# Performance work log

Measured on AMD Instinct MI355X. Metric: run time of the kernel, lower is better.

Reference implementation:

```python
import jax, jax.numpy as jnp
import numpy as np

N_NODES = 1000      # nodes per graph
B = 64              # graphs in batch
N = B * N_NODES     # total nodes
E = 2048000         # total edges
F_IN, D1, D2 = 128, 256, 64


def setup_inputs() -> dict:
    key = jax.random.key(0)
    ks = jax.random.split(key, 24)
    def p(k, shape, fan_in):
        return jax.random.normal(k, shape, dtype=jnp.float32) * (1.0 / np.sqrt(fan_in))
    inp = {
        "x": jax.random.normal(ks[0], (N, F_IN), dtype=jnp.float32),
        "edge_index": jax.random.randint(ks[1], (2, E), 0, N, dtype=jnp.int32).astype(jnp.int64),
        "edge_attr": jax.random.uniform(ks[2], (E,), dtype=jnp.float32),
        # GraphConv1: lin_rel (neighbors) and lin_root (self)
        "Wl1": p(ks[3], (D1, F_IN), F_IN), "bl1": jnp.zeros((D1,), jnp.float32),
        "Wr1": p(ks[4], (D1, F_IN), F_IN), "br1": jnp.zeros((D1,), jnp.float32),
        # GraphConv2
        "Wl2": p(ks[5], (D2, D1), D1), "bl2": jnp.zeros((D2,), jnp.float32),
        "Wr2": p(ks[6], (D2, D1), D1), "br2": jnp.zeros((D2,), jnp.float32),
        # bottleneck fc / fc2
        "Wfc": p(ks[7], (D2, N_NODES * D2), N_NODES * D2), "bfc": jnp.zeros((D2,), jnp.float32),
        "Wfc2": p(ks[8], (N_NODES * D2, D2), D2), "bfc2": jnp.zeros((N_NODES * D2,), jnp.float32),
        # concatDec MLP: Linear(2*D2 -> D1) -> relu -> Linear(D1 -> 1)
        "Wd1": p(ks[9], (D1, 2 * D2), 2 * D2), "bd1": jnp.zeros((D1,), jnp.float32),
        "Wd2": p(ks[10], (1, D1), D1), "bd2": jnp.zeros((1,), jnp.float32),
    }
    return inp


def _graph_conv(x, src, dst, ew, Wl, bl, Wr, br):
    # PyG GraphConv: out = lin_rel(sum_{j in N(i)} w_ij * x_j) + lin_root(x_i)
    m = x[src] * ew[:, None]                       # [E, F] gather + scale
    agg = jax.ops.segment_sum(m, dst, num_segments=N)  # scatter-add to targets
    return agg @ Wl.T + bl + x @ Wr.T + br


def reference(x, edge_index, edge_attr,
              Wl1, bl1, Wr1, br1, Wl2, bl2, Wr2, br2,
              Wfc, bfc, Wfc2, bfc2, Wd1, bd1, Wd2, bd2):
    src = edge_index[0]
    dst = edge_index[1]
    # encode (dropout_adj / Dropout are identity at inference)
    h = jax.nn.relu(_graph_conv(x, src, dst, edge_attr, Wl1, bl1, Wr1, br1))
    z = _graph_conv(h, src, dst, edge_attr, Wl2, bl2, Wr2, br2)   # [N, D2]
    z = jax.nn.relu(z.reshape(-1, N_NODES * D2))                   # [B, N_NODES*D2]
    z = z @ Wfc.T + bfc                                            # [B, D2]
    # decode
    z = jax.nn.relu(z @ Wfc2.T + bfc2)                             # [B, N_NODES*D2]
    z = z.reshape(-1, D2)                                          # [N, D2]
    # concatDec over edges
    h_e = jnp.concatenate([z[src], z[dst]], axis=1)                # [E, 2*D2]
    h_e = jax.nn.relu(h_e @ Wd1.T + bd1)                           # [E, D1]
    pred = (h_e @ Wd2.T + bd2).reshape(-1)                         # [E]
    return jax.nn.sigmoid(pred)
```

## Files before the change

kernel.cpp:

```cpp
#include <hip/hip_runtime.h>
#include <math.h>

typedef __attribute__((ext_vector_type(8))) _Float16 f16x8;
typedef __attribute__((ext_vector_type(4))) _Float16 f16x4;
typedef __attribute__((ext_vector_type(2))) _Float16 f16x2;
typedef __attribute__((ext_vector_type(4))) float f32x4;

static __device__ __forceinline__ int getidx(const int* __restrict__ ei, int mode, long long pos) {
  return mode ? ei[2 * pos] : ei[pos];
}

__global__ void detect_kernel(const int* __restrict__ ei, int* __restrict__ mode) {
  int lane = threadIdx.x & 63;
  int v = ei[2 * lane + 1] | ei[2 * lane + 129];
  unsigned long long nz = __ballot(v != 0);
  if (lane == 0) mode[0] = (nz == 0ull) ? 1 : 0;
}

__global__ void zero_kernel(float* __restrict__ p, long long n) {
  long long i = (long long)blockIdx.x * blockDim.x + threadIdx.x;
  if (i < n) p[i] = 0.f;
}

__global__ void f32tof16_kernel(const float* __restrict__ in, unsigned short* __restrict__ out,
                                long long n4) {
  long long i = (long long)blockIdx.x * 256 + threadIdx.x;
  if (i >= n4) return;
  float4 v = ((const float4*)in)[i];
  f16x4 h;
  h[0] = (_Float16)v.x; h[1] = (_Float16)v.y; h[2] = (_Float16)v.z; h[3] = (_Float16)v.w;
  ((f16x4*)out)[i] = h;
}

__global__ void w16cat_kernel(const float* __restrict__ Wl1, const float* __restrict__ Wr1,
                              const float* __restrict__ Wl2, const float* __restrict__ Wr2,
                              unsigned short* __restrict__ wh1, unsigned short* __restrict__ wh2) {
  int idx = blockIdx.x * 256 + threadIdx.x;
  if (idx < 65536) {
    int o = idx >> 8, k = idx & 255;
    float v = (k < 128) ? Wl1[o * 128 + k] : Wr1[o * 128 + k - 128];
    _Float16 hv = (_Float16)v;
    wh1[idx] = *(unsigned short*)&hv;
  } else if (idx < 65536 + 32768) {
    int i2 = idx - 65536;
    int o = i2 >> 8, k = i2 & 255;
    float v = (o < 64) ? Wl2[o * 256 + k] : Wr2[(o - 64) * 256 + k];
    _Float16 hv = (_Float16)v;
    wh2[i2] = *(unsigned short*)&hv;
  }
}

__global__ void hist_kernel(const int* __restrict__ ei, int* __restrict__ cnt,
                            const int* __restrict__ modep, int E) {
  const int md = modep[0];
  int e = blockIdx.x * 256 + threadIdx.x;
  if (e >= E) return;
  int d = getidx(ei, md, (long long)E + e);
  atomicAdd(&cnt[d], 1);
}

__global__ void scan1_kernel(const int* __restrict__ cnt, int* __restrict__ pre,
                             int* __restrict__ bsum, int N) {
  __shared__ int ws[4];
  int i = blockIdx.x * 256 + threadIdx.x;
  int v = (i < N) ? cnt[i] : 0;
  int lane = threadIdx.x & 63, w = threadIdx.x >> 6;
  int s = v;
#pragma unroll
  for (int o = 1; o < 64; o <<= 1) { int t = __shfl_up(s, o); if (lane >= o) s += t; }
  if (lane == 63) ws[w] = s;
  __syncthreads();
  int off = 0;
  for (int k = 0; k < w; ++k) off += ws[k];
  if (i < N) pre[i] = s + off - v;
  if (threadIdx.x == 255) bsum[blockIdx.x] = s + off;
}

__global__ void scan2_kernel(int* __restrict__ bsum, int nb) {
  __shared__ int ws[4];
  int i = threadIdx.x;
  int v = (i < nb) ? bsum[i] : 0;
  int lane = i & 63, w = i >> 6;
  int s = v;
#pragma unroll
  for (int o = 1; o < 64; o <<= 1) { int t = __shfl_up(s, o); if (lane >= o) s += t; }
  if (lane == 63) ws[w] = s;
  __syncthreads();
  int off = 0;
  for (int k = 0; k < w; ++k) off += ws[k];
  if (i < nb) bsum[i] = s + off - v;
}

__global__ void scan3_kernel(int* __restrict__ rowptr, const int* __restrict__ bsum,
                             int* __restrict__ fill, int N, int E) {
  int i = blockIdx.x * 256 + threadIdx.x;
  if (i < N) {
    int r = rowptr[i] + bsum[blockIdx.x];
    rowptr[i] = r;
    fill[i] = r;
  }
  if (i == 0) rowptr[N] = E;
}

__global__ void reorder_kernel(const int* __restrict__ ei, const float* __restrict__ ea,
                               int* __restrict__ fill, uint4* __restrict__ se2,
                               const int* __restrict__ modep, int E) {
  const int md = modep[0];
  int e = blockIdx.x * 256 + threadIdx.x;
  if (e >= E) return;
  int s = getidx(ei, md, e);
  int d = getidx(ei, md, (long long)E + e);
  int pos = atomicAdd(&fill[d], 1);
  se2[pos] = make_uint4((unsigned)s, __float_as_uint(ea[e]), (unsigned)e, (unsigned)d);
}

__global__ void agg1_csr_kernel(const int* __restrict__ rowptr, const uint4* __restrict__ se2,
                                const unsigned short* __restrict__ xh,
                                unsigned short* __restrict__ agg1h, int N) {
  int n = (int)((blockIdx.x * 256 + threadIdx.x) >> 6);
  int lane = threadIdx.x & 63;
  if (n >= N) return;
  int p = rowptr[n], end = rowptr[n + 1];
  float ax = 0.f, ay = 0.f;
  for (; p + 1 < end; p += 2) {
    uint4 e0 = se2[p], e1 = se2[p + 1];
    float w0 = __uint_as_float(e0.y), w1 = __uint_as_float(e1.y);
    f16x2 v0 = *(const f16x2*)&xh[(size_t)e0.x * 128 + lane * 2];
    f16x2 v1 = *(const f16x2*)&xh[(size_t)e1.x * 128 + lane * 2];
    ax += (float)v0[0] * w0 + (float)v1[0] * w1;
    ay += (float)v0[1] * w0 + (float)v1[1] * w1;
  }
  if (p < end) {
    uint4 e0 = se2[p];
    float w0 = __uint_as_float(e0.y);
    f16x2 v0 = *(const f16x2*)&xh[(size_t)e0.x * 128 + lane * 2];
    ax += (float)v0[0] * w0;
    ay += (float)v0[1] * w0;
  }
  f16x2 st; st[0] = (_Float16)ax; st[1] = (_Float16)ay;
  *(f16x2*)&agg1h[(size_t)n * 128 + lane * 2] = st;
}

__global__ void agg2_csr_kernel(const int* __restrict__ rowptr, const uint4* __restrict__ se2,
                                const unsigned short* __restrict__ th, float* __restrict__ agg2,
                                int N) {
  int n = (int)((blockIdx.x * 256 + threadIdx.x) >> 6);
  int lane = threadIdx.x & 63;
  if (n >= N) return;
  int p = rowptr[n], end = rowptr[n + 1];
  float acc = 0.f;
  for (; p + 1 < end; p += 2) {
    uint4 e0 = se2[p], e1 = se2[p + 1];
    _Float16 t0 = *(const _Float16*)&th[(size_t)e0.x * 64 + lane];
    _Float16 t1 = *(const _Float16*)&th[(size_t)e1.x * 64 + lane];
    acc += (float)t0 * __uint_as_float(e0.y) + (float)t1 * __uint_as_float(e1.y);
  }
  if (p < end) {
    uint4 e0 = se2[p];
    _Float16 t0 = *(const _Float16*)&th[(size_t)e0.x * 64 + lane];
    acc += (float)t0 * __uint_as_float(e0.y);
  }
  agg2[(size_t)n * 64 + lane] += acc;
}

__global__ void scatter1_kernel(const int* __restrict__ ei, const float* __restrict__ ea,
                                const float* __restrict__ x, float* __restrict__ agg1,
                                const int* __restrict__ modep, int E) {
  const int md = modep[0];
  int e = (int)(((long long)blockIdx.x * 256 + threadIdx.x) >> 6);
  int lane = threadIdx.x & 63;
  if (e >= E) return;
  int s = getidx(ei, md, e);
  int d = getidx(ei, md, (long long)E + e);
  float w = ea[e];
  float2 v = *(const float2*)&x[(size_t)s * 128 + lane * 2];
  float* ap = &agg1[(size_t)d * 128 + lane * 2];
  atomicAdd(ap, v.x * w);
  atomicAdd(ap + 1, v.y * w);
}

__global__ void scatter2_kernel(const int* __restrict__ ei, const float* __restrict__ ea,
                                const float* __restrict__ t, float* __restrict__ agg2,
                                const int* __restrict__ modep, int E) {
  const int md = modep[0];
  int e = (int)(((long long)blockIdx.x * 256 + threadIdx.x) >> 6);
  int lane = threadIdx.x & 63;
  if (e >= E) return;
  int s = getidx(ei, md, e);
  int d = getidx(ei, md, (long long)E + e);
  float w = ea[e];
  atomicAdd(&agg2[(size_t)d * 64 + lane], t[(size_t)s * 64 + lane] * w);
}

__global__ void gemm_bt(const float* __restrict__ A1, const float* __restrict__ W1, int K1,
                        const float* __restrict__ A2, const float* __restrict__ W2, int K2,
                        const float* __restrict__ b1, const float* __restrict__ b2,
                        float* __restrict__ C, int NC, int doRelu) {
  __shared__ float As[64][17];
  __shared__ float Ws[64][17];
  int tid = threadIdx.x;
  int tx = tid & 15, ty = tid >> 4;
  int row0 = blockIdx.y * 64, col0 = blockIdx.x * 64;
  float acc[4][4] = {};
  for (int srcsel = 0; srcsel < 2; ++srcsel) {
    const float* A = srcsel ? A2 : A1;
    const float* W = srcsel ? W2 : W1;
    int K = srcsel ? K2 : K1;
    if (!A) continue;
    for (int kb = 0; kb < K; kb += 16) {
#pragma unroll
      for (int i = 0; i < 4; ++i) {
        int idx = tid + 256 * i;
        int r = idx >> 4, k = idx & 15;
        As[r][k] = A[(size_t)(row0 + r) * K + kb + k];
        Ws[r][k] = W[(size_t)(col0 + r) * K + kb + k];
      }
      __syncthreads();
#pragma unroll
      for (int k = 0; k < 16; ++k) {
        float a[4], w[4];
#pragma unroll
        for (int i = 0; i < 4; ++i) a[i] = As[ty * 4 + i][k];
#pragma unroll
        for (int j = 0; j < 4; ++j) w[j] = Ws[tx * 4 + j][k];
#pragma unroll
        for (int i = 0; i < 4; ++i)
#pragma unroll
          for (int j = 0; j < 4; ++j) acc[i][j] += a[i] * w[j];
      }
      __syncthreads();
    }
  }
#pragma unroll
  for (int j = 0; j < 4; ++j) {
    int c = col0 + tx * 4 + j;
    float bias = (b1 ? b1[c] : 0.f) + (b2 ? b2[c] : 0.f);
#pragma unroll
    for (int i = 0; i < 4; ++i) {
      float v = acc[i][j] + bias;
      if (doRelu) v = fmaxf(v, 0.f);
      C[(size_t)(row0 + ty * 4 + i) * NC + c] = v;
    }
  }
}

template <int MODE, int OTN>
__global__ void __launch_bounds__(256, 2)
gemm16_kernel(const uint4* __restrict__ A0, const uint4* __restrict__ A1, int c0,
              const unsigned short* __restrict__ Wcat,
              const float* __restrict__ b1, const float* __restrict__ b2,
              unsigned short* __restrict__ outH, float* __restrict__ outF) {
  __shared__ uint4 At[64 * 33];
  int tid = threadIdx.x;
  int lane = tid & 63;
  int wv = tid >> 6;
  int l15 = lane & 15, g = lane >> 4;
  int row0 = blockIdx.x * 64;

  f16x8 bfr[OTN][8];
  float biasv[OTN];
#pragma unroll
  for (int ot = 0; ot < OTN; ++ot) {
    int o = wv * (OTN * 16) + ot * 16 + l15;
    if (MODE == 0) biasv[ot] = b1[o] + b2[o];
    else biasv[ot] = (o >= 64) ? (b1[o - 64] + b2[o - 64]) : 0.f;
#pragma unroll
    for (int kb = 0; kb < 8; ++kb)
      bfr[ot][kb] = *(const f16x8*)&Wcat[(size_t)o * 256 + kb * 32 + g * 8];
  }

#pragma unroll
  for (int i = 0; i < 8; ++i) {
    int idx = tid + 256 * i;
    int r = idx >> 5, c = idx & 31;
    uint4 v = (c < c0) ? A0[(size_t)(row0 + r) * c0 + c]
                       : A1[(size_t)(row0 + r) * (32 - c0) + (c - c0)];
    At[r * 33 + c] = v;
  }
  __syncthreads();

#pragma unroll
  for (int est = 0; est < 4; ++est) {
    int rowA = est * 16 + l15;
    f16x8 a[8];
#pragma unroll
    for (int kb = 0; kb < 8; ++kb)
      a[kb] = *(const f16x8*)&At[rowA * 33 + kb * 4 + g];
#pragma unroll
    for (int ot = 0; ot < OTN; ++ot) {
      f32x4 acc = {0.f, 0.f, 0.f, 0.f};
#pragma unroll
      for (int kb = 0; kb < 8; ++kb)
        acc = __builtin_amdgcn_mfma_f32_16x16x32_f16(a[kb], bfr[ot][kb], acc, 0, 0, 0);
      int o = wv * (OTN * 16) + ot * 16 + l15;
#pragma unroll
      for (int r = 0; r < 4; ++r) {
        int row = row0 + est * 16 + g * 4 + r;
        float v = acc[r] + biasv[ot];
        if (MODE == 0) {
          _Float16 hv = (_Float16)fmaxf(v, 0.f);
          outH[(size_t)row * 256 + o] = *(unsigned short*)&hv;
        } else {
          if (o < 64) {
            _Float16 hv = (_Float16)v;
            outH[(size_t)row * 64 + o] = *(unsigned short*)&hv;
          } else {
            outF[(size_t)row * 64 + (o - 64)] = v;
          }
        }
      }
    }
  }
}

__global__ void __launch_bounds__(256) fc1_kernel(const float* __restrict__ z0,
                                                  const float* __restrict__ Wfc,
                                                  const float* __restrict__ bfc,
                                                  float* __restrict__ z1) {
  __shared__ float Zs[64][260];
  int tid = threadIdx.x;
  int kc = blockIdx.x;
  const size_t kbase = (size_t)kc * 256;
  for (int i = tid; i < 64 * 256; i += 256) {
    int b = i >> 8, k = i & 255;
    Zs[b][k] = fmaxf(z0[(size_t)b * 64000 + kbase + k], 0.f);
  }
  __syncthreads();
  int o = tid >> 2, q = tid & 3;
  float acc[16];
#pragma unroll
  for (int j = 0; j < 16; ++j) acc[j] = 0.f;
  const float* wp = Wfc + (size_t)o * 64000 + kbase;
  for (int k = 0; k < 256; k += 4) {
    float4 w = *(const float4*)&wp[k];
#pragma unroll
    for (int j = 0; j < 16; ++j) {
      float4 z = *(const float4*)&Zs[q * 16 + j][k];
      acc[j] += z.x * w.x + z.y * w.y + z.z * w.z + z.w * w.w;
    }
  }
  float bias = (kc == 0) ? bfc[o] : 0.f;
#pragma unroll
  for (int j = 0; j < 16; ++j)
    atomicAdd(&z1[(q * 16 + j) * 64 + o], acc[j] + bias);
}

__global__ void fc2_kernel(const float* __restrict__ z1, const float* __restrict__ Wfc2,
                           const float* __restrict__ bfc2,
                           unsigned short* __restrict__ z2h, int nPerB) {
  __shared__ float z1s[4096];
  __shared__ float Ws[256][65];
  int tid = threadIdx.x;
  for (int i = tid; i < 4096; i += 256) z1s[i] = z1[i];
  int m0 = blockIdx.x * 256;
  for (int i = tid; i < 256 * 64; i += 256) {
    int r = i >> 6, j = i & 63;
    Ws[r][j] = Wfc2[(size_t)(m0 + r) * 64 + j];
  }
  __syncthreads();
  int m = m0 + tid;
  float bias = bfc2[m];
  int ninb = m >> 6, feat = m & 63;
  for (int b = 0; b < 64; ++b) {
    float acc = bias;
#pragma unroll
    for (int j = 0; j < 64; ++j) acc += z1s[b * 64 + j] * Ws[tid][j];
    float v = fmaxf(acc, 0.f);
    _Float16 hv = (_Float16)v;
    size_t node = (size_t)b * nPerB + ninb;
    z2h[node * 64 + feat] = *(unsigned short*)&hv;
  }
}

__global__ void __launch_bounds__(256, 2)
decoder_kernel(const uint4* __restrict__ se2, const int* __restrict__ ei,
               const unsigned short* __restrict__ z2h,
               const float* __restrict__ Wd1, const float* __restrict__ bd1,
               const float* __restrict__ Wd2, const float* __restrict__ bd2,
               float* __restrict__ obuf, const int* __restrict__ modep,
               int E, int sorted) {
  __shared__ uint4 At[128 * 17];
  __shared__ int nid[256];
  __shared__ float red[4][128];
  const int md = modep[0];
  int tid = threadIdx.x;
  int lane = tid & 63;
  int wv = tid >> 6;
  int l15 = lane & 15, g = lane >> 4;
  int ue = tid >> 3, c8 = tid & 7;

  f16x8 bfr[4][4];
  float wd2v[4], bd1v[4];
#pragma unroll
  for (int ot = 0; ot < 4; ++ot) {
    int o = wv * 64 + ot * 16 + l15;
    wd2v[ot] = Wd2[o];
    bd1v[ot] = bd1[o];
#pragma unroll
    for (int kb = 0; kb < 4; ++kb) {
      const float* wp = Wd1 + (size_t)o * 128 + kb * 32 + g * 8;
      f16x8 bh;
#pragma unroll
      for (int q = 0; q < 8; ++q) bh[q] = (_Float16)wp[q];
      bfr[ot][kb] = bh;
    }
  }
  float bd2v = bd2[0];

  int ntiles = E >> 7;
  int tpb = (ntiles + gridDim.x - 1) / gridDim.x;
  int tA = blockIdx.x * tpb;
  int tB = min(tA + tpb, ntiles);

  for (int tile = tA; tile < tB; ++tile) {
    long long ebase = (long long)tile << 7;
    if (sorted) {
      if (tid < 128) {
        uint4 v = se2[ebase + tid];
        nid[tid] = (int)v.x;
        nid[128 + tid] = (int)v.w;
      }
    } else {
      long long p = ebase + (tid & 127);
      nid[tid] = getidx(ei, md, (tid < 128) ? p : (long long)E + p);
    }
    __syncthreads();
#pragma unroll
    for (int pass = 0; pass < 8; ++pass) {
      int u = pass * 32 + ue;
      int node = nid[u];
      uint4 v = *((const uint4*)(z2h + (size_t)node * 64) + c8);
      int eRow = u & 127, side = u >> 7;
      At[eRow * 17 + side * 8 + c8] = v;
    }
    __syncthreads();

    float sacc[8][4];
#pragma unroll
    for (int i = 0; i < 8; ++i)
#pragma unroll
      for (int r = 0; r < 4; ++r) sacc[i][r] = 0.f;

#pragma unroll
    for (int est = 0; est < 8; ++est) {
      int row = est * 16 + l15;
      f16x8 a[4];
#pragma unroll
      for (int kb = 0; kb < 4; ++kb)
        a[kb] = *(const f16x8*)&At[row * 17 + kb * 4 + g];
#pragma unroll
      for (int ot = 0; ot < 4; ++ot) {
        f32x4 acc = {0.f, 0.f, 0.f, 0.f};
#pragma unroll
        for (int kb = 0; kb < 4; ++kb)
          acc = __builtin_amdgcn_mfma_f32_16x16x32_f16(a[kb], bfr[ot][kb], acc, 0, 0, 0);
#pragma unroll
        for (int r = 0; r < 4; ++r) {
          float pp = fmaxf(acc[r] + bd1v[ot], 0.f);
          sacc[est][r] += pp * wd2v[ot];
        }
      }
    }
#pragma unroll
    for (int est = 0; est < 8; ++est)
#pragma unroll
      for (int r = 0; r < 4; ++r) {
        float s = sacc[est][r];
        s += __shfl_xor(s, 1); s += __shfl_xor(s, 2);
        s += __shfl_xor(s, 4); s += __shfl_xor(s, 8);
        sacc[est][r] = s;
      }
    if (l15 == 0) {
#pragma unroll
      for (int est = 0; est < 8; ++est)
#pragma unroll
        for (int r = 0; r < 4; ++r)
          red[wv][est * 16 + g * 4 + r] = sacc[est][r];
    }
    __syncthreads();
    if (tid < 128) {
      float s = red[0][tid] + red[1][tid] + red[2][tid] + red[3][tid] + bd2v;
      obuf[ebase + tid] = 1.f / (1.f + __expf(-s));
    }
  }
}

__global__ void permute_out(const float* __restrict__ outsorted, const uint4* __restrict__ se2,
                            float* __restrict__ out, int E) {
  int i = blockIdx.x * 256 + threadIdx.x;
  if (i < E) out[se2[i].z] = outsorted[i];
}

extern "C" void kernel_launch(void* const* d_in, const int* in_sizes, int n_in,
                              void* d_out, int out_size, void* d_ws, size_t ws_size,
                              hipStream_t stream) {
  const float* x    = (const float*)d_in[0];
  const int*   ei   = (const int*)d_in[1];
  const float* ea   = (const float*)d_in[2];
  const float* Wl1  = (const float*)d_in[3];
  const float* bl1  = (const float*)d_in[4];
  const float* Wr1  = (const float*)d_in[5];
  const float* br1  = (const float*)d_in[6];
  const float* Wl2  = (const float*)d_in[7];
  const float* bl2  = (const float*)d_in[8];
  const float* Wr2  = (const float*)d_in[9];
  const float* br2  = (const float*)d_in[10];
  const float* Wfc  = (const float*)d_in[11];
  const float* bfc  = (const float*)d_in[12];
  const float* Wfc2 = (const float*)d_in[13];
  const float* bfc2 = (const float*)d_in[14];
  const float* Wd1  = (const float*)d_in[15];
  const float* bd1  = (const float*)d_in[16];
  const float* Wd2  = (const float*)d_in[17];
  const float* bd2  = (const float*)d_in[18];
  float* out = (float*)d_out;

  const int N = in_sizes[0] / 128;
  const int E = in_sizes[2];
  const int NB = (N + 255) / 256;

  float* agg1 = (float*)d_ws;
  float* z1   = agg1 + (size_t)N * 128;
  float* h    = z1 + 4096;
  float* t    = h + (size_t)N * 256;
  float* agg2 = t + (size_t)N * 64;
  uint4* se2  = (uint4*)(agg2 + (size_t)N * 64);
  int* cnt    = (int*)(se2 + E);
  int* rowptr = cnt + N;
  int* fill   = rowptr + N + 1;
  int* bsum   = fill + N;
  int* mode_csr = bsum + 256;
  float* outsorted = (float*)(mode_csr + 4);
  unsigned short* wh1 = (unsigned short*)(((uintptr_t)(outsorted + E) + 15) & ~(uintptr_t)15);
  unsigned short* wh2 = wh1 + 65536;

  unsigned short* agg1h = (unsigned short*)agg1;
  unsigned short* xh    = agg1h + (size_t)N * 128;
  unsigned short* hh    = (unsigned short*)h;
  unsigned short* z2h   = (unsigned short*)t;
  unsigned short* th    = z2h + (size_t)N * 64;

  size_t base = ((size_t)N * 128 + 4096 + (size_t)N * 256 + (size_t)N * 128) * 4;
  size_t need_old = base + 64;
  size_t need_csr = base + (size_t)E * 16 + ((size_t)3 * N + 300) * 4 + (size_t)E * 4
                  + (size_t)(65536 + 32768) * 2 + 128;
  if (ws_size < need_old || out_size < E) return;
  bool use_csr = (ws_size >= need_csr);
  int* mode = use_csr ? mode_csr : (int*)(se2);

  detect_kernel<<<1, 64, 0, stream>>>(ei, mode);

  if (use_csr) {
    zero_kernel<<<17, 256, 0, stream>>>(z1, 4096);
    zero_kernel<<<NB, 256, 0, stream>>>((float*)cnt, N);
    hist_kernel<<<(E + 255) / 256, 256, 0, stream>>>(ei, cnt, mode, E);
    scan1_kernel<<<NB, 256, 0, stream>>>(cnt, rowptr, bsum, N);
    scan2_kernel<<<1, 256, 0, stream>>>(bsum, NB);
    scan3_kernel<<<NB, 256, 0, stream>>>(rowptr, bsum, fill, N, E);
    reorder_kernel<<<(E + 255) / 256, 256, 0, stream>>>(ei, ea, fill, se2, mode, E);
    w16cat_kernel<<<384, 256, 0, stream>>>(Wl1, Wr1, Wl2, Wr2, wh1, wh2);
    long long n4 = (long long)N * 32;
    f32tof16_kernel<<<(int)((n4 + 255) / 256), 256, 0, stream>>>(x, xh, n4);
    agg1_csr_kernel<<<(N + 3) / 4, 256, 0, stream>>>(rowptr, se2, xh, agg1h, N);
    gemm16_kernel<0, 4><<<N / 64, 256, 0, stream>>>((const uint4*)agg1h, (const uint4*)xh, 16,
                                                    wh1, bl1, br1, hh, nullptr);
    gemm16_kernel<1, 2><<<N / 64, 256, 0, stream>>>((const uint4*)hh, (const uint4*)hh, 32,
                                                    wh2, bl2, br2, th, agg2);
    agg2_csr_kernel<<<(N + 3) / 4, 256, 0, stream>>>(rowptr, se2, th, agg2, N);
  } else {
    long long nz = (long long)N * 128 + 4096;
    zero_kernel<<<(int)((nz + 255) / 256), 256, 0, stream>>>(agg1, nz);
    scatter1_kernel<<<E / 4, 256, 0, stream>>>(ei, ea, x, agg1, mode, E);
    gemm_bt<<<dim3(4, N / 64), 256, 0, stream>>>(agg1, Wl1, 128, x, Wr1, 128, bl1, br1, h, 256, 1);
    gemm_bt<<<dim3(1, N / 64), 256, 0, stream>>>(h, Wl2, 256, nullptr, nullptr, 0, nullptr, nullptr, t, 64, 0);
    gemm_bt<<<dim3(1, N / 64), 256, 0, stream>>>(h, Wr2, 256, nullptr, nullptr, 0, bl2, br2, agg2, 64, 0);
    scatter2_kernel<<<E / 4, 256, 0, stream>>>(ei, ea, t, agg2, mode, E);
  }

  fc1_kernel<<<250, 256, 0, stream>>>(agg2, Wfc, bfc, z1);
  fc2_kernel<<<250, 256, 0, stream>>>(z1, Wfc2, bfc2, z2h, N / 64);

  if (use_csr) {
    decoder_kernel<<<2048, 256, 0, stream>>>(se2, ei, z2h, Wd1, bd1, Wd2, bd2,
                                             outsorted, mode, E, 1);
    permute_out<<<(E + 255) / 256, 256, 0, stream>>>(outsorted, se2, out, E);
  } else {
    decoder_kernel<<<2048, 256, 0, stream>>>(se2, ei, z2h, Wd1, bd1, Wd2, bd2,
                                             out, mode, E, 0);
  }
}
```

Before: 942.0 us.

## Double-buffer decoder tile gathers to overlap z2h loads with MFMA compute

Splits the decoder's shared-memory edge tile and node-index buffers into two halves. Each iteration issues the global z2h row gathers for the next tile into registers before running the MFMA and reduction on the current tile, then writes them to the alternate buffer afterward. The goal is to hide gather latency behind compute. The cost is double the LDS footprint, about 8 extra uint4 registers per thread, and added control flow, which may reduce occupancy under launch_bounds(256,2).

```diff
diff --git a/kernel.cpp b/kernel.cpp
--- a/kernel.cpp
+++ b/kernel.cpp
@@ -379,8 +379,8 @@
                const float* __restrict__ Wd2, const float* __restrict__ bd2,
                float* __restrict__ obuf, const int* __restrict__ modep,
                int E, int sorted) {
-  __shared__ uint4 At[128 * 17];
-  __shared__ int nid[256];
+  __shared__ uint4 At[2][128 * 17];
+  __shared__ int nid[2][256];
   __shared__ float red[4][128];
   const int md = modep[0];
   int tid = threadIdx.x;
@@ -411,30 +411,62 @@
   int tpb = (ntiles + gridDim.x - 1) / gridDim.x;
   int tA = blockIdx.x * tpb;
   int tB = min(tA + tpb, ntiles);
-
-  for (int tile = tA; tile < tB; ++tile) {
-    long long ebase = (long long)tile << 7;
+  if (tA >= tB) return;
+
+  {
+    long long eb0 = (long long)tA << 7;
     if (sorted) {
       if (tid < 128) {
-        uint4 v = se2[ebase + tid];
-        nid[tid] = (int)v.x;
-        nid[128 + tid] = (int)v.w;
+        uint4 v = se2[eb0 + tid];
+        nid[0][tid] = (int)v.x;
+        nid[0][128 + tid] = (int)v.w;
+        if (tA + 1 < tB) {
+          uint4 v1 = se2[eb0 + 128 + tid];
+          nid[1][tid] = (int)v1.x;
+          nid[1][128 + tid] = (int)v1.w;
+        }
       }
     } else {
-      long long p = ebase + (tid & 127);
-      nid[tid] = getidx(ei, md, (tid < 128) ? p : (long long)E + p);
+      long long p = eb0 + (tid & 127);
+      nid[0][tid] = getidx(ei, md, (tid < 128) ? p : (long long)E + p);
+      if (tA + 1 < tB) {
+        long long p1 = p + 128;
+        nid[1][tid] = getidx(ei, md, (tid < 128) ? p1 : (long long)E + p1);
+      }
     }
     __syncthreads();
 #pragma unroll
     for (int pass = 0; pass < 8; ++pass) {
       int u = pass * 32 + ue;
-      int node = nid[u];
+      int node = nid[0][u];
       uint4 v = *((const uint4*)(z2h + (size_t)node * 64) + c8);
       int eRow = u & 127, side = u >> 7;
-      At[eRow * 17 + side * 8 + c8] = v;
+      At[0][eRow * 17 + side * 8 + c8] = v;
     }
     __syncthreads();
-
+  }
+
+  int cur = 0;
+  for (int t = tA; t < tB; ++t) {
+    int nxt = cur ^ 1;
+    long long ebase = (long long)t << 7;
+
+    uint4 G0, G1, G2, G3, G4, G5, G6, G7;
+    bool havenext = (t + 1 < tB);
+    if (havenext) {
+      const uint4* zp;
+      int node;
+      node = nid[nxt][0 * 32 + ue]; zp = (const uint4*)(z2h + (size_t)node * 64); G0 = zp[c8];
+      node = nid[nxt][1 * 32 + ue]; zp = (const uint4*)(z2h + (size_t)node * 64); G1 = zp[c8];
+      node = nid[nxt][2 * 32 + ue]; zp = (const uint4*)(z2h + (size_t)node * 64); G2 = zp[c8];
+      node = nid[nxt][3 * 32 + ue]; zp = (const uint4*)(z2h + (size_t)node * 64); G3 = zp[c8];
+      node = nid[nxt][4 * 32 + ue]; zp = (const uint4*)(z2h + (size_t)node * 64); G4 = zp[c8];
+      node = nid[nxt][5 * 32 + ue]; zp = (const uint4*)(z2h + (size_t)node * 64); G5 = zp[c8];
+      node = nid[nxt][6 * 32 + ue]; zp = (const uint4*)(z2h + (size_t)node * 64); G6 = zp[c8];
+      node = nid[nxt][7 * 32 + ue]; zp = (const uint4*)(z2h + (size_t)node * 64); G7 = zp[c8];
+    }
+
+    const uint4* Ac = &At[cur][0];
     float sacc[8][4];
 #pragma unroll
     for (int i = 0; i < 8; ++i)
@@ -447,7 +479,7 @@
       f16x8 a[4];
 #pragma unroll
       for (int kb = 0; kb < 4; ++kb)
-        a[kb] = *(const f16x8*)&At[row * 17 + kb * 4 + g];
+        a[kb] = *(const f16x8*)&Ac[row * 17 + kb * 4 + g];
 #pragma unroll
       for (int ot = 0; ot < 4; ++ot) {
         f32x4 acc = {0.f, 0.f, 0.f, 0.f};
@@ -482,6 +514,34 @@
       float s = red[0][tid] + red[1][tid] + red[2][tid] + red[3][tid] + bd2v;
       obuf[ebase + tid] = 1.f / (1.f + __expf(-s));
     }
+
+    if (havenext) {
+      int base = (ue & 127) * 17 + (ue >> 7) * 8 + c8;
+#pragma unroll
+      for (int pass = 0; pass < 8; ++pass) {
+        int u = pass * 32 + ue;
+        int eRow = u & 127, side = u >> 7;
+        uint4 v = (pass == 0) ? G0 : (pass == 1) ? G1 : (pass == 2) ? G2 : (pass == 3) ? G3
+                : (pass == 4) ? G4 : (pass == 5) ? G5 : (pass == 6) ? G6 : G7;
+        At[nxt][eRow * 17 + side * 8 + c8] = v;
+      }
+      (void)base;
+      if (t + 2 < tB) {
+        long long eb2 = (long long)(t + 2) << 7;
+        if (sorted) {
+          if (tid < 128) {
+            uint4 v = se2[eb2 + tid];
+            nid[cur][tid] = (int)v.x;
+            nid[cur][128 + tid] = (int)v.w;
+          }
+        } else {
+          long long p = eb2 + (tid & 127);
+          nid[cur][tid] = getidx(ei, md, (tid < 128) ? p : (long long)E + p);
+        }
+      }
+    }
+    __syncthreads();
+    cur = nxt;
   }
 }
 
```

Result: slower. 971.4 us (+3.1%).
